# Kernel optimization log

Hardware: AMD Instinct MI355X
Metric: run time of the kernel (lower is better)

## Reference

```python
import jax, jax.numpy as jnp
import numpy as np

K = 4
TEMP = 34.0
KS = 3
PAD = 1
STRIDE = 1


def setup_inputs() -> dict:
    key = jax.random.key(0)
    k0, k1, k2, k3, k4, k5 = jax.random.split(key, 6)
    B, C, H, W = 32, 256, 56, 56
    OC = 256
    HID = int(C * 0.25) + 1  # 65
    x = jax.random.normal(k0, (B, C, H, W), jnp.float32)
    # kaiming-ish scales for the 1x1 attention convs (treated as matmuls)
    w_fc1 = jax.random.normal(k1, (HID, C), jnp.float32) * np.float32(np.sqrt(2.0 / C))
    w_fc2 = jax.random.normal(k2, (K, HID), jnp.float32) * np.float32(np.sqrt(2.0 / HID))
    b_fc2 = jnp.zeros((K,), jnp.float32)
    # positive step sizes for numerical sanity (torch inits randn then overwrites at init_state)
    alpha = jax.random.uniform(k3, (K, 1), jnp.float32, minval=0.05, maxval=1.0)
    weight = jax.random.normal(k4, (K, OC, C, KS, KS), jnp.float32) * 0.05
    bias_w = jax.random.normal(k5, (K, OC), jnp.float32) * 0.01
    return dict(x=x, w_fc1=w_fc1, w_fc2=w_fc2, b_fc2=b_fc2, alpha=alpha,
                weight=weight, bias_w=bias_w)


def _round_ste(v):
    # round_pass: forward round, backward identity
    return v + jax.lax.stop_gradient(jnp.round(v) - v)


def _lsq_quant(w2d, alpha):
    # Faithful to the torch LSQQuantizer forward (eval path): divide by per-row
    # alpha, clamp ONLY scalar elements [0,0],[1,0],[2,0] (as the torch code does),
    # then straight-through round and rescale. grad_scale copies into .data and
    # therefore has no effect on values or the autograd graph.
    d = w2d / alpha  # (K, M)
    d = d.at[0, 0].set(jnp.clip(d[0, 0], -2.0, 1.0))   # 2-bit range
    d = d.at[1, 0].set(jnp.clip(d[1, 0], -4.0, 3.0))   # 3-bit range
    d = d.at[2, 0].set(jnp.clip(d[2, 0], -8.0, 7.0))   # 4-bit range
    return _round_ste(d) * alpha


def reference(x, w_fc1, w_fc2, b_fc2, alpha, weight, bias_w):
    B, C, H, W = x.shape
    Kk, OC = bias_w.shape
    # attention2d: global avg pool -> 1x1 conv -> relu -> 1x1 conv (+bias)
    pooled = x.mean(axis=(2, 3))                     # (B, C)
    h = jax.nn.relu(pooled @ w_fc1.T)                # (B, HID)
    raw = h @ w_fc2.T + b_fc2                        # (B, K)
    # gradient_approximation: forward = one-hot(argmax), backward = softmax(x/T)
    soft = jax.nn.softmax(raw / TEMP, axis=1)
    hard = jax.nn.one_hot(jnp.argmax(raw, axis=1), Kk, dtype=raw.dtype)
    attn = soft + jax.lax.stop_gradient(hard - soft)  # (B, K)
    # LSQ-quantize flattened expert weights, then per-sample aggregation
    wq = _lsq_quant(weight.reshape(Kk, -1), alpha)   # (K, OC*C*KS*KS)
    agg_w = (attn @ wq).reshape(B, OC, C, KS, KS)    # per-sample kernels
    agg_b = attn @ bias_w                            # (B, OC)
    # per-sample conv2d (equivalent to the groups=batch trick)
    def conv1(xb, wb):
        return jax.lax.conv_general_dilated(
            xb[None], wb, (STRIDE, STRIDE), [(PAD, PAD), (PAD, PAD)],
            dimension_numbers=('NCHW', 'OIHW', 'NCHW'))[0]
    out = jax.vmap(conv1)(x, agg_w) + agg_b[:, :, None, None]  # (B, OC, H, W)
    return (out, raw)
```

## Files before the change

kernel.cpp:

```cpp
#include <hip/hip_runtime.h>
#include <hip/hip_bf16.h>

typedef __attribute__((ext_vector_type(8))) short short8;
typedef __attribute__((ext_vector_type(4))) float f32x4;

#define XPAD_OFF   0u
#define WQ_OFF     62717952u
#define POOL_OFF   67436544u
#define IDX_OFF    67469312u

__device__ __forceinline__ void gl_lds16(const void* g, void* l) {
  __builtin_amdgcn_global_load_lds(
      (const __attribute__((address_space(1))) unsigned int*)g,
      (__attribute__((address_space(3))) unsigned int*)l, 16, 0, 0);
}

__global__ __launch_bounds__(128) void fc_argmax_kernel(
    const float* __restrict__ pooled, const float* __restrict__ w_fc1,
    const float* __restrict__ w_fc2, const float* __restrict__ b_fc2,
    float* __restrict__ raw_out, int* __restrict__ idx) {
  __shared__ float h[65];
  __shared__ float raws[4];
  const int b = blockIdx.x, t = threadIdx.x;
  if (t < 65) {
    float s = 0.f;
    const float* pb = pooled + b * 256;
    const float* wr = w_fc1 + t * 256;
    for (int c = 0; c < 256; ++c) s += pb[c] * wr[c];
    s *= (1.0f / 3136.0f);
    h[t] = s > 0.f ? s : 0.f;
  }
  __syncthreads();
  if (t < 4) {
    float s = b_fc2[t];
    const float* wr = w_fc2 + t * 65;
    for (int j = 0; j < 65; ++j) s += h[j] * wr[j];
    raws[t] = s;
    raw_out[b * 4 + t] = s;
  }
  __syncthreads();
  if (t == 0) {
    int best = 0; float bv = raws[0];
    for (int k = 1; k < 4; ++k) if (raws[k] > bv) { bv = raws[k]; best = k; }
    idx[b] = best;
  }
}

__global__ __launch_bounds__(256) void quant_kernel(
    const float* __restrict__ weight, const float* __restrict__ alpha,
    __hip_bfloat16* __restrict__ Wq) {
  const unsigned d = blockIdx.x * 256u + threadIdx.x;
  const unsigned cl   = d & 7u;
  const unsigned lane = (d >> 3) & 63u;
  const unsigned arow = lane & 15u;
  const unsigned kgrp = lane >> 4;
  const unsigned i    = (d >> 9) & 3u;
  const unsigned wm   = (d >> 11) & 1u;
  const unsigned cb32 = (d >> 12) & 7u;
  const unsigned rest = d >> 15;
  const unsigned tap  = rest % 9u;
  const unsigned q    = rest / 9u;
  const unsigned ot   = q & 1u;
  const unsigned k    = q >> 1;
  const unsigned oc = ot * 128u + wm * 64u + i * 16u + arow;
  const unsigned ch = cb32 * 32u + kgrp * 8u + cl;
  const float a = alpha[k];
  float v = weight[(size_t)k * 589824u + oc * 2304u + ch * 9u + tap] / a;
  if (oc == 0u && ch == 0u && tap == 0u) {
    if (k == 0u)      v = fminf(fmaxf(v, -2.f), 1.f);
    else if (k == 1u) v = fminf(fmaxf(v, -4.f), 3.f);
    else if (k == 2u) v = fminf(fmaxf(v, -8.f), 7.f);
  }
  Wq[d] = __float2bfloat16(rintf(v) * a);
}

__global__ __launch_bounds__(256) void padx_kernel(const float* __restrict__ x,
                                                   __hip_bfloat16* __restrict__ Xpad,
                                                   float* __restrict__ pooled) {
  __shared__ float T[56 * 132];
  const int yp = blockIdx.x;
  const int c0 = blockIdx.y * 128;
  const int b  = blockIdx.z;
  const int tid = threadIdx.x;
  __hip_bfloat16* orow = Xpad + ((size_t)(b * 58 + yp) * 66) * 256 + c0;
  const short8 zero8 = (short8){0, 0, 0, 0, 0, 0, 0, 0};
  const bool rowin = (yp >= 1 && yp <= 56);
  if (rowin) {
    const float* xbase = x + (((size_t)b * 256 + c0) * 56 + (yp - 1)) * 56;
    for (int i = tid; i < 128 * 56; i += 256) {
      const int cl = i / 56, px = i - cl * 56;
      T[px * 132 + cl] = xbase[cl * 3136 + px];
    }
    __syncthreads();
    if (tid < 128) {
      float s = 0.f;
      for (int px = 0; px < 56; ++px) s += T[px * 132 + tid];
      atomicAdd(pooled + b * 256 + c0 + tid, s);
    }
    for (int i = tid; i < 896; i += 256) {
      const int px = i >> 4, cg = (i & 15) * 8;
      union { short8 v; __hip_bfloat16 e[8]; } u;
      #pragma unroll
      for (int r = 0; r < 8; ++r) u.e[r] = __float2bfloat16(T[px * 132 + cg + r]);
      *(short8*)&orow[(px + 1) * 256 + cg] = u.v;
    }
    for (int i = tid; i < 160; i += 256) {
      const int pi = i >> 4, cg = (i & 15) * 8;
      const int xp = (pi == 0) ? 0 : 56 + pi;
      *(short8*)&orow[xp * 256 + cg] = zero8;
    }
  } else {
    for (int i = tid; i < 66 * 16; i += 256) {
      const int xp = i >> 4, cg = (i & 15) * 8;
      *(short8*)&orow[xp * 256 + cg] = zero8;
    }
  }
}

__global__ __launch_bounds__(256, 4) void conv_kernel(
    const __hip_bfloat16* __restrict__ Xpad, const __hip_bfloat16* __restrict__ Wq,
    const int* __restrict__ idx, const float* __restrict__ bias_w,
    float* __restrict__ out) {
  __shared__ __attribute__((aligned(16))) __hip_bfloat16 Xs[17408];

  const int tid = threadIdx.x;
  const int lane = tid & 63;
  const int w = tid >> 6;
  const int wm = w & 1;
  const int wn = w >> 1;

  const int pt = blockIdx.x;
  const int ot = blockIdx.y;
  const int b = blockIdx.z;
  const int Y0 = pt * 2;
  const int OC0 = ot * 128;
  const int kb = idx[b];

  const __hip_bfloat16* xb = Xpad + (size_t)b * (58 * 66 * 256);
  const short8* W0 = (const short8*)Wq + (size_t)(kb * 2 + ot) * 36864;

  f32x4 acc[4][4];
  #pragma unroll
  for (int i = 0; i < 4; ++i)
    #pragma unroll
    for (int j = 0; j < 4; ++j) acc[i][j] = (f32x4){0.f, 0.f, 0.f, 0.f};

  const int arow = lane & 15;
  const int kgrp = lane >> 4;

  auto stage = [&](int cbh, int bufsel) {
    char* dst = (char*)Xs + bufsel * 17408;
    for (int k = w; k < 17; k += 4) {
      const int s = k * 64 + lane;
      int p = s >> 2;
      if (p > 263) p = 263;
      const int g = (s & 3) ^ ((p >> 1) & 3);
      const int r = p / 66, xc = p - r * 66;
      gl_lds16(xb + (((Y0 + r) * 66 + xc) * 256 + cbh * 32 + g * 8),
               dst + k * 1024);
    }
  };

  stage(0, 0);
  __syncthreads();

  short8 af[4], afn[4];
  #pragma unroll
  for (int i = 0; i < 4; ++i)
    af[i] = W0[(size_t)(wm * 256) + i * 64 + lane];

  for (int cbh = 0; cbh < 8; ++cbh) {
    const __hip_bfloat16* cur = Xs + (cbh & 1) * 8704;
    if (cbh < 7) stage(cbh + 1, (cbh + 1) & 1);

    #pragma unroll
    for (int tap = 0; tap < 9; ++tap) {
      const int dy = tap / 3, dx = tap - dy * 3;
      short8 bfr[4];
      #pragma unroll
      for (int j = 0; j < 4; ++j) {
        const int p = (wn + dy) * 66 + j * 16 + arow + dx;
        const int slot = p * 4 + (kgrp ^ ((p >> 1) & 3));
        bfr[j] = *(const short8*)&cur[slot * 8];
      }
      if (tap < 8) {
        #pragma unroll
        for (int i = 0; i < 4; ++i)
          afn[i] = W0[(((tap + 1) * 8 + cbh) * 2 + wm) * 256 + i * 64 + lane];
      } else if (cbh < 7) {
        #pragma unroll
        for (int i = 0; i < 4; ++i)
          afn[i] = W0[((cbh + 1) * 2 + wm) * 256 + i * 64 + lane];
      }
      #pragma unroll
      for (int i = 0; i < 4; ++i)
        #pragma unroll
        for (int j = 0; j < 4; ++j)
          acc[i][j] = __builtin_amdgcn_mfma_f32_16x16x32_bf16(
              af[i], bfr[j], acc[i][j], 0, 0, 0);
      #pragma unroll
      for (int i = 0; i < 4; ++i) af[i] = afn[i];
    }
    __syncthreads();
  }

  const float* biasb = bias_w + kb * 256 + OC0;
  #pragma unroll
  for (int i = 0; i < 4; ++i) {
    const int ocbase = wm * 64 + i * 16 + (lane >> 4) * 4;
    #pragma unroll
    for (int j = 0; j < 4; ++j) {
      const int pl = wn * 64 + j * 16 + (lane & 15);
      const int xcol = pl & 63;
      if (xcol < 56) {
        const int y = Y0 + (pl >> 6);
        #pragma unroll
        for (int r = 0; r < 4; ++r) {
          const int oc = ocbase + r;
          out[(((size_t)b * 256 + OC0 + oc) * 56 + y) * 56 + xcol] =
              acc[i][j][r] + biasb[oc];
        }
      }
    }
  }
}

extern "C" void kernel_launch(void* const* d_in, const int* in_sizes, int n_in,
                              void* d_out, int out_size, void* d_ws, size_t ws_size,
                              hipStream_t stream) {
  const float* x      = (const float*)d_in[0];
  const float* w_fc1  = (const float*)d_in[1];
  const float* w_fc2  = (const float*)d_in[2];
  const float* b_fc2  = (const float*)d_in[3];
  const float* alpha  = (const float*)d_in[4];
  const float* weight = (const float*)d_in[5];
  const float* bias_w = (const float*)d_in[6];

  float* out = (float*)d_out;
  float* raw_out = out + (size_t)32 * 256 * 56 * 56;

  char* ws = (char*)d_ws;
  __hip_bfloat16* Xpad = (__hip_bfloat16*)(ws + XPAD_OFF);
  __hip_bfloat16* Wq   = (__hip_bfloat16*)(ws + WQ_OFF);
  float* pooled        = (float*)(ws + POOL_OFF);
  int* idx             = (int*)(ws + IDX_OFF);

  hipMemsetAsync(pooled, 0, 32 * 256 * sizeof(float), stream);
  padx_kernel<<<dim3(58, 2, 32), 256, 0, stream>>>(x, Xpad, pooled);
  quant_kernel<<<9216, 256, 0, stream>>>(weight, alpha, Wq);
  fc_argmax_kernel<<<32, 128, 0, stream>>>(pooled, w_fc1, w_fc2, b_fc2, raw_out, idx);
  conv_kernel<<<dim3(28, 2, 32), 256, 0, stream>>>(Xpad, Wq, idx, bias_w, out);
}
```

Measured before the change: 372.5 us.

## Switch conv to 32x32x16 MFMA with 4-row tiles and interleaved staging

Replaces the 16x16x32 MFMA tiling with 32x32x16 bf16 MFMAs over 128 OC by 4 output rows per block, which halves the grid. The quantized weight layout and the padded-X row width (66 down to 58) change to match. Async LDS staging of the next channel chunk is now spread across the tap loop, and weights are prefetched two taps ahead with a triple register buffer. The aim is fewer LDS reads per FLOP and better MFMA efficiency, at the cost of larger LDS use and lower occupancy (launch bounds 2).

```diff
diff --git a/kernel.cpp b/kernel.cpp
--- a/kernel.cpp
+++ b/kernel.cpp
@@ -2,12 +2,12 @@
 #include <hip/hip_bf16.h>
 
 typedef __attribute__((ext_vector_type(8))) short short8;
-typedef __attribute__((ext_vector_type(4))) float f32x4;
+typedef __attribute__((ext_vector_type(16))) float f32x16;
 
 #define XPAD_OFF   0u
-#define WQ_OFF     62717952u
-#define POOL_OFF   67436544u
-#define IDX_OFF    67469312u
+#define WQ_OFF     55115776u
+#define POOL_OFF   59834368u
+#define IDX_OFF    59867136u
 
 __device__ __forceinline__ void gl_lds16(const void* g, void* l) {
   __builtin_amdgcn_global_load_lds(
@@ -51,19 +51,21 @@
     __hip_bfloat16* __restrict__ Wq) {
   const unsigned d = blockIdx.x * 256u + threadIdx.x;
   const unsigned cl   = d & 7u;
-  const unsigned lane = (d >> 3) & 63u;
-  const unsigned arow = lane & 15u;
-  const unsigned kgrp = lane >> 4;
-  const unsigned i    = (d >> 9) & 3u;
-  const unsigned wm   = (d >> 11) & 1u;
-  const unsigned cb32 = (d >> 12) & 7u;
-  const unsigned rest = d >> 15;
-  const unsigned tap  = rest % 9u;
-  const unsigned q    = rest / 9u;
+  const unsigned g    = d >> 3;
+  const unsigned lane = g & 63u;
+  const unsigned u    = g >> 6;
+  const unsigned low  = u & 63u;
+  const unsigned s      = low & 1u;
+  const unsigned octile = (low >> 1) & 1u;
+  const unsigned wm     = (low >> 2) & 1u;
+  const unsigned cbh    = (low >> 3) & 7u;
+  const unsigned t6   = u >> 6;
+  const unsigned tap  = t6 % 9u;
+  const unsigned q    = t6 / 9u;
   const unsigned ot   = q & 1u;
   const unsigned k    = q >> 1;
-  const unsigned oc = ot * 128u + wm * 64u + i * 16u + arow;
-  const unsigned ch = cb32 * 32u + kgrp * 8u + cl;
+  const unsigned oc = ot * 128u + wm * 64u + octile * 32u + (lane & 31u);
+  const unsigned ch = cbh * 32u + s * 16u + (lane >> 5) * 8u + cl;
   const float a = alpha[k];
   float v = weight[(size_t)k * 589824u + oc * 2304u + ch * 9u + tap] / a;
   if (oc == 0u && ch == 0u && tap == 0u) {
@@ -82,7 +84,7 @@
   const int c0 = blockIdx.y * 128;
   const int b  = blockIdx.z;
   const int tid = threadIdx.x;
-  __hip_bfloat16* orow = Xpad + ((size_t)(b * 58 + yp) * 66) * 256 + c0;
+  __hip_bfloat16* orow = Xpad + ((size_t)(b * 58 + yp) * 58) * 256 + c0;
   const short8 zero8 = (short8){0, 0, 0, 0, 0, 0, 0, 0};
   const bool rowin = (yp >= 1 && yp <= 56);
   if (rowin) {
@@ -104,24 +106,24 @@
       for (int r = 0; r < 8; ++r) u.e[r] = __float2bfloat16(T[px * 132 + cg + r]);
       *(short8*)&orow[(px + 1) * 256 + cg] = u.v;
     }
-    for (int i = tid; i < 160; i += 256) {
-      const int pi = i >> 4, cg = (i & 15) * 8;
-      const int xp = (pi == 0) ? 0 : 56 + pi;
+    for (int i = tid; i < 32; i += 256) {
+      const int cg = (i & 15) * 8;
+      const int xp = (i >> 4) ? 57 : 0;
       *(short8*)&orow[xp * 256 + cg] = zero8;
     }
   } else {
-    for (int i = tid; i < 66 * 16; i += 256) {
+    for (int i = tid; i < 58 * 16; i += 256) {
       const int xp = i >> 4, cg = (i & 15) * 8;
       *(short8*)&orow[xp * 256 + cg] = zero8;
     }
   }
 }
 
-__global__ __launch_bounds__(256, 4) void conv_kernel(
+__global__ __launch_bounds__(256, 2) void conv_kernel(
     const __hip_bfloat16* __restrict__ Xpad, const __hip_bfloat16* __restrict__ Wq,
     const int* __restrict__ idx, const float* __restrict__ bias_w,
     float* __restrict__ out) {
-  __shared__ __attribute__((aligned(16))) __hip_bfloat16 Xs[17408];
+  __shared__ __attribute__((aligned(16))) __hip_bfloat16 Xs[22784];
 
   const int tid = threadIdx.x;
   const int lane = tid & 63;
@@ -132,93 +134,98 @@
   const int pt = blockIdx.x;
   const int ot = blockIdx.y;
   const int b = blockIdx.z;
-  const int Y0 = pt * 2;
+  const int Y0 = pt * 4;
   const int OC0 = ot * 128;
   const int kb = idx[b];
 
-  const __hip_bfloat16* xb = Xpad + (size_t)b * (58 * 66 * 256);
+  const __hip_bfloat16* xb = Xpad + (size_t)b * (58 * 58 * 256);
   const short8* W0 = (const short8*)Wq + (size_t)(kb * 2 + ot) * 36864;
 
-  f32x4 acc[4][4];
+  f32x16 acc[2][4];
   #pragma unroll
-  for (int i = 0; i < 4; ++i)
-    #pragma unroll
-    for (int j = 0; j < 4; ++j) acc[i][j] = (f32x4){0.f, 0.f, 0.f, 0.f};
-
-  const int arow = lane & 15;
-  const int kgrp = lane >> 4;
-
-  auto stage = [&](int cbh, int bufsel) {
-    char* dst = (char*)Xs + bufsel * 17408;
-    for (int k = w; k < 17; k += 4) {
-      const int s = k * 64 + lane;
-      int p = s >> 2;
-      if (p > 263) p = 263;
-      const int g = (s & 3) ^ ((p >> 1) & 3);
-      const int r = p / 66, xc = p - r * 66;
-      gl_lds16(xb + (((Y0 + r) * 66 + xc) * 256 + cbh * 32 + g * 8),
-               dst + k * 1024);
-    }
+  for (int i = 0; i < 2; ++i)
+    #pragma unroll
+    for (int j = 0; j < 4; ++j)
+      acc[i][j] = (f32x16){0,0,0,0,0,0,0,0,0,0,0,0,0,0,0,0};
+
+  const int nlo = lane & 31;
+  const int khalf = lane >> 5;
+
+  auto stageseg = [&](int cbn, int bufsel, int k) {
+    int sidx = k * 64 + lane;
+    int p = sidx >> 2;
+    if (p > 347) p = 347;
+    const int gsel = (sidx & 3) ^ ((p >> 1) & 3);
+    const int r = p / 58, xc = p - r * 58;
+    gl_lds16(xb + (((Y0 + r) * 58 + xc) * 256 + cbn * 32 + gsel * 8),
+             (char*)Xs + bufsel * 22784 + k * 1024);
   };
 
-  stage(0, 0);
+  for (int k = w; k < 22; k += 4) stageseg(0, 0, k);
   __syncthreads();
 
-  short8 af[4], afn[4];
+  short8 afr[3][4];
   #pragma unroll
-  for (int i = 0; i < 4; ++i)
-    af[i] = W0[(size_t)(wm * 256) + i * 64 + lane];
+  for (int oc2 = 0; oc2 < 2; ++oc2)
+    #pragma unroll
+    for (int s2 = 0; s2 < 2; ++s2) {
+      afr[0][oc2 * 2 + s2] = W0[0 * 4096 + 0 * 512 + wm * 256 + oc2 * 128 + s2 * 64 + lane];
+      afr[1][oc2 * 2 + s2] = W0[1 * 4096 + 0 * 512 + wm * 256 + oc2 * 128 + s2 * 64 + lane];
+    }
 
   for (int cbh = 0; cbh < 8; ++cbh) {
-    const __hip_bfloat16* cur = Xs + (cbh & 1) * 8704;
-    if (cbh < 7) stage(cbh + 1, (cbh + 1) & 1);
-
-    #pragma unroll
-    for (int tap = 0; tap < 9; ++tap) {
-      const int dy = tap / 3, dx = tap - dy * 3;
-      short8 bfr[4];
+    const __hip_bfloat16* cur = Xs + (cbh & 1) * 11392;
+    const int nb = (cbh + 1) & 1;
+
+    #pragma unroll
+    for (int t = 0; t < 9; ++t) {
+      const int dy = t / 3, dx = t - dy * 3;
+      if (cbh < 7) {
+        if (t < 5) stageseg(cbh + 1, nb, w + 4 * t);
+        else if (t == 5 && w < 2) stageseg(cbh + 1, nb, w + 20);
+      }
+      if (cbh < 7 || t < 7) {
+        const int tap2 = (t + 2) % 9, cb2 = cbh + (t + 2) / 9;
+        #pragma unroll
+        for (int oc2 = 0; oc2 < 2; ++oc2)
+          #pragma unroll
+          for (int s2 = 0; s2 < 2; ++s2)
+            afr[(t + 2) % 3][oc2 * 2 + s2] =
+                W0[tap2 * 4096 + cb2 * 512 + wm * 256 + oc2 * 128 + s2 * 64 + lane];
+      }
       #pragma unroll
-      for (int j = 0; j < 4; ++j) {
-        const int p = (wn + dy) * 66 + j * 16 + arow + dx;
-        const int slot = p * 4 + (kgrp ^ ((p >> 1) & 3));
-        bfr[j] = *(const short8*)&cur[slot * 8];
-      }
-      if (tap < 8) {
+      for (int s = 0; s < 2; ++s) {
         #pragma unroll
-        for (int i = 0; i < 4; ++i)
-          afn[i] = W0[(((tap + 1) * 8 + cbh) * 2 + wm) * 256 + i * 64 + lane];
-      } else if (cbh < 7) {
+        for (int j = 0; j < 4; ++j) {
+          const int row = wn * 2 + (j >> 1) + dy;
+          const int col = (j & 1) * 32 + nlo + dx;
+          const int p = row * 58 + col;
+          const int slot = p * 4 + ((s * 2 + khalf) ^ ((p >> 1) & 3));
+          const short8 bfr = *(const short8*)&cur[slot * 8];
+          #pragma unroll
+          for (int i = 0; i < 2; ++i)
+            acc[i][j] = __builtin_amdgcn_mfma_f32_32x32x16_bf16(
+                afr[t % 3][i * 2 + s], bfr, acc[i][j], 0, 0, 0);
+        }
+      }
+    }
+    __syncthreads();
+  }
+
+  const float* biasb = bias_w + kb * 256;
+  #pragma unroll
+  for (int i = 0; i < 2; ++i) {
+    #pragma unroll
+    for (int j = 0; j < 4; ++j) {
+      const int xcol = (j & 1) * 32 + nlo;
+      if (xcol < 56) {
+        const int y = Y0 + wn * 2 + (j >> 1);
         #pragma unroll
-        for (int i = 0; i < 4; ++i)
-          afn[i] = W0[((cbh + 1) * 2 + wm) * 256 + i * 64 + lane];
-      }
-      #pragma unroll
-      for (int i = 0; i < 4; ++i)
-        #pragma unroll
-        for (int j = 0; j < 4; ++j)
-          acc[i][j] = __builtin_amdgcn_mfma_f32_16x16x32_bf16(
-              af[i], bfr[j], acc[i][j], 0, 0, 0);
-      #pragma unroll
-      for (int i = 0; i < 4; ++i) af[i] = afn[i];
-    }
-    __syncthreads();
-  }
-
-  const float* biasb = bias_w + kb * 256 + OC0;
-  #pragma unroll
-  for (int i = 0; i < 4; ++i) {
-    const int ocbase = wm * 64 + i * 16 + (lane >> 4) * 4;
-    #pragma unroll
-    for (int j = 0; j < 4; ++j) {
-      const int pl = wn * 64 + j * 16 + (lane & 15);
-      const int xcol = pl & 63;
-      if (xcol < 56) {
-        const int y = Y0 + (pl >> 6);
-        #pragma unroll
-        for (int r = 0; r < 4; ++r) {
-          const int oc = ocbase + r;
-          out[(((size_t)b * 256 + OC0 + oc) * 56 + y) * 56 + xcol] =
-              acc[i][j][r] + biasb[oc];
+        for (int reg = 0; reg < 16; ++reg) {
+          const int row = (reg & 3) + 8 * (reg >> 2) + 4 * khalf;
+          const int oc = OC0 + wm * 64 + i * 32 + row;
+          out[(((size_t)b * 256 + oc) * 56 + y) * 56 + xcol] =
+              acc[i][j][reg] + biasb[oc];
         }
       }
     }
@@ -249,5 +256,5 @@
   padx_kernel<<<dim3(58, 2, 32), 256, 0, stream>>>(x, Xpad, pooled);
   quant_kernel<<<9216, 256, 0, stream>>>(weight, alpha, Wq);
   fc_argmax_kernel<<<32, 128, 0, stream>>>(pooled, w_fc1, w_fc2, b_fc2, raw_out, idx);
-  conv_kernel<<<dim3(28, 2, 32), 256, 0, stream>>>(Xpad, Wq, idx, bias_w, out);
-}
+  conv_kernel<<<dim3(14, 2, 32), 256, 0, stream>>>(Xpad, Wq, idx, bias_w, out);
+}
```

Result: faster. 336.5 us (-9.7%).
